# Kernel tuning notes

Hardware: AMD Instinct MI355X
Metric: run time of the kernel (lower is better)

Reference implementation:

```python
import jax, jax.numpy as jnp
import numpy as np

B, TXT_T, MEL_T, N_MEL = 8, 200, 800, 80
PAD_MAG = 1.0e12


def setup_inputs() -> dict:
    key = jax.random.key(0)
    k1, k2, k3, k4 = jax.random.split(key, 4)
    mu_logvar = jax.random.normal(k1, (B, TXT_T, 2 * N_MEL), dtype=jnp.float32)
    melspec = jax.random.normal(k2, (B, N_MEL, MEL_T), dtype=jnp.float32)
    # lengths are 1-based (indexed as length-1), keep them in [T//2, T]
    text_lengths = jax.random.randint(k3, (B,), TXT_T // 2, TXT_T + 1)
    mel_lengths = jax.random.randint(k4, (B,), MEL_T // 2, MEL_T + 1)
    return {
        "mu_logvar": mu_logvar,
        "melspec": melspec,
        "text_lengths": text_lengths,
        "mel_lengths": mel_lengths,
    }


def _log_prob_matrix(mu_logvar, melspec):
    # melspec: [B, n_mel, mel_T] -> x: [B, 1, mel_T, n_mel]
    x = jnp.transpose(melspec, (0, 2, 1))[:, None, :, :]
    mu = mu_logvar[:, :, :N_MEL][:, :, None, :]       # [B, txt_T, 1, n_mel]
    logvar = mu_logvar[:, :, N_MEL:][:, :, None, :]   # [B, txt_T, 1, n_mel]
    # -0.5 * mean_over_mel( (x-mu)^2 / exp(logvar) + logvar )
    sq = (x - mu) ** 2
    return (-0.5 * (sq * jnp.exp(-logvar) + logvar)).mean(axis=3)  # [B, txt_T, mel_T]


def reference(mu_logvar, melspec, text_lengths, mel_lengths):
    lp = _log_prob_matrix(mu_logvar, melspec)  # [B, txt_T, mel_T]

    # log_alpha column carry, with a leading pad row (index 0 stays -PAD_MAG)
    init = jnp.full((B, TXT_T + 1), -PAD_MAG, dtype=lp.dtype)
    init = init.at[:, 1].set(lp[:, 0, 0])

    def step(a, lp_t):  # a: [B, txt_T+1], lp_t: [B, txt_T]
        # logsumexp over {stay, advance}; original adds 1e-7 to prev values
        new_rows = jnp.logaddexp(a[:, 1:] + 1e-7, a[:, :-1] + 1e-7) + lp_t
        a = a.at[:, 1:].set(new_rows)
        return a, new_rows

    lp_rest = jnp.moveaxis(lp[:, :, 1:], 2, 0)  # [mel_T-1, B, txt_T]
    _, cols = jax.lax.scan(step, init, lp_rest)  # cols: [mel_T-1, B, txt_T]

    log_alpha = jnp.concatenate(
        [init[:, 1:, None], jnp.moveaxis(cols, 0, 2)], axis=2
    )  # [B, txt_T, mel_T]

    b = jnp.arange(B)
    alpha_last = log_alpha[b, text_lengths - 1, mel_lengths - 1]
    alpha_last = alpha_last / mel_lengths.astype(alpha_last.dtype)
    mdn_loss = -alpha_last.mean()
    return mdn_loss, lp
```

## Files before the change

kernel.cpp:

```cpp
#include <hip/hip_runtime.h>
#include <math.h>

#define BB 8
#define TXT_T 200
#define MEL_T 800
#define N_MEL 80
#define NTHR 192
#define LOG2E 1.44269504088896340736f
#define LN2   0.69314718055994530942f
#define EPS2  (1e-7f * LOG2E)
#define NPAD  -1.0e12f

__device__ __forceinline__ float exp2_hw(float x) {
#if __has_builtin(__builtin_amdgcn_exp2f)
    return __builtin_amdgcn_exp2f(x);
#else
    return __expf(LN2 * x);
#endif
}

__device__ __forceinline__ float lse2(float A, float B) {
    float m = fmaxf(A, B);
    float e = exp2_hw(-fabsf(A - B));
    return m + __log2f(1.0f + e);
}

template <int D>
__device__ __forceinline__ float dpp_shr(float v, float old) {
#if __has_builtin(__builtin_amdgcn_update_dpp)
    return __int_as_float(__builtin_amdgcn_update_dpp(
        __float_as_int(old), __float_as_int(v), 0x110 | D, 0xF, 0xF, false));
#else
    float t = __shfl_up(v, D);
    return ((threadIdx.x & 15) < D) ? old : t;
#endif
}

__global__ void __launch_bounds__(256) lp_kernel(
        const float* __restrict__ mu_logvar,
        const float* __restrict__ melspec,
        float* __restrict__ out_lp,
        float* __restrict__ lpT) {
    const int bt = blockIdx.x;
    const int b  = bt / TXT_T;
    const int tid = threadIdx.x;

    __shared__ float s_mu[N_MEL];
    __shared__ float s_ev[N_MEL];
    __shared__ float s_lv[N_MEL];
    __shared__ float s_sumlv;

    if (tid < N_MEL) {
        float mu = mu_logvar[(size_t)bt * (2 * N_MEL) + tid];
        float lv = mu_logvar[(size_t)bt * (2 * N_MEL) + N_MEL + tid];
        s_mu[tid] = mu;
        s_ev[tid] = __expf(-lv);
        s_lv[tid] = lv;
    }
    __syncthreads();
    if (tid == 0) {
        float s = 0.f;
        #pragma unroll
        for (int n = 0; n < N_MEL; ++n) s += s_lv[n];
        s_sumlv = s;
    }
    __syncthreads();

    if (tid < MEL_T / 4) {
        const float4* ms4 = (const float4*)(melspec + (size_t)b * N_MEL * MEL_T);
        float ax = 0.f, ay = 0.f, az = 0.f, aw = 0.f;
        #pragma unroll 8
        for (int n = 0; n < N_MEL; ++n) {
            float4 x = ms4[(size_t)n * (MEL_T / 4) + tid];
            float mu = s_mu[n];
            float ev = s_ev[n];
            float d0 = x.x - mu; ax += d0 * d0 * ev;
            float d1 = x.y - mu; ay += d1 * d1 * ev;
            float d2 = x.z - mu; az += d2 * d2 * ev;
            float d3 = x.w - mu; aw += d3 * d3 * ev;
        }
        const float c = -0.5f / (float)N_MEL;
        float slv = s_sumlv;
        float l0 = c * (ax + slv);
        float l1 = c * (ay + slv);
        float l2 = c * (az + slv);
        float l3 = c * (aw + slv);

        size_t ob = (size_t)bt * MEL_T + tid * 4;
        out_lp[ob + 0] = l0;
        out_lp[ob + 1] = l1;
        out_lp[ob + 2] = l2;
        out_lp[ob + 3] = l3;

        float4 v;
        v.x = l0 * LOG2E + EPS2;
        v.y = l1 * LOG2E + EPS2;
        v.z = l2 * LOG2E + EPS2;
        v.w = l3 * LOG2E + EPS2;
        *(float4*)(lpT + ob) = v;
    }
}

__global__ void __launch_bounds__(NTHR) scan_kernel(
        const float* __restrict__ lpT,
        const int* __restrict__ text_lengths,
        const int* __restrict__ mel_lengths,
        float* __restrict__ alpha_out) {
    __shared__ float tot[2][4][2];
    const int b = blockIdx.x;
    const int tid = threadIdx.x;
    const int w = tid >> 6;
    const int lane = tid & 63;

    const int melL1 = mel_lengths[b] - 1;
    const int txtL1 = text_lengths[b] - 1;
    const float scale = LN2 / (float)(melL1 + 1);
    const int estar = melL1 - txtL1;
    const int gtid = estar >> 2;
    const int gk = estar & 3;

    const float* cb = lpT + (size_t)b * TXT_T * MEL_T;

    float A0 = (tid == 0) ? -EPS2 : NPAD;
    float A1 = NPAD, A2 = NPAD, A3 = NPAD;

    #define LDCOL(JN, L0, L1, L2, L3) do {                                    \
        int jn_ = (JN);                                                       \
        const float* cp_ = cb + (size_t)jn_ * MEL_T;                          \
        int t0_ = jn_ + 4 * tid;                                              \
        int i0_ = t0_ + 0 > 799 ? 799 : t0_ + 0;                              \
        int i1_ = t0_ + 1 > 799 ? 799 : t0_ + 1;                              \
        int i2_ = t0_ + 2 > 799 ? 799 : t0_ + 2;                              \
        int i3_ = t0_ + 3 > 799 ? 799 : t0_ + 3;                              \
        L0 = cp_[i0_]; L1 = cp_[i1_]; L2 = cp_[i2_]; L3 = cp_[i3_];           \
    } while (0)

    float p0, p1, p2, p3, n0, n1, n2, n3;
    LDCOL(0, p0, p1, p2, p3);
    LDCOL(txtL1 >= 1 ? 1 : 0, n0, n1, n2, n3);

    int par = 0;
    for (int j = 0; j <= txtL1; ++j) {
        float al0 = p0, al1 = p1, al2 = p2, al3 = p3;
        p0 = n0; p1 = n1; p2 = n2; p3 = n3;
        {
            int jn = j + 2 > txtL1 ? txtL1 : j + 2;
            LDCOL(jn, n0, n1, n2, n3);
        }

        float be0 = al0 + A0;
        float be1 = al1 + A1;
        float be2 = al2 + A2;
        float be3 = al3 + A3;

        float I0a = al0,        I0b = be0;
        float I1a = al1 + I0a,  I1b = lse2(al1 + I0b, be1);
        float t23a = al3 + al2, t23b = lse2(al3 + be2, be3);
        float I2a = al2 + I1a,  I2b = lse2(al2 + I1b, be2);
        float I3a = t23a + I1a, I3b = lse2(t23a + I1b, t23b);

        float Ta = I3a, Tb = I3b;
        {
            float ia, ib;
            ia = dpp_shr<1>(Ta, 0.0f); ib = dpp_shr<1>(Tb, NPAD);
            Tb = lse2(Ta + ib, Tb); Ta = Ta + ia;
            ia = dpp_shr<2>(Ta, 0.0f); ib = dpp_shr<2>(Tb, NPAD);
            Tb = lse2(Ta + ib, Tb); Ta = Ta + ia;
            ia = dpp_shr<4>(Ta, 0.0f); ib = dpp_shr<4>(Tb, NPAD);
            Tb = lse2(Ta + ib, Tb); Ta = Ta + ia;
            ia = dpp_shr<8>(Ta, 0.0f); ib = dpp_shr<8>(Tb, NPAD);
            Tb = lse2(Ta + ib, Tb); Ta = Ta + ia;
        }

        float t0a = __shfl(Ta, 15), t0b = __shfl(Tb, 15);
        float t1a = __shfl(Ta, 31), t1b = __shfl(Tb, 31);
        float t2a = __shfl(Ta, 47), t2b = __shfl(Tb, 47);
        float c2a = t1a + t0a, c2b = lse2(t1a + t0b, t1b);
        float c3a = t2a + c2a, c3b = lse2(t2a + c2b, t2b);
        int row = lane >> 4;
        float Xa = 0.0f, Xb = NPAD;
        if (row == 1) { Xa = t0a; Xb = t0b; }
        if (row == 2) { Xa = c2a; Xb = c2b; }
        if (row == 3) { Xa = c3a; Xb = c3b; }
        float Fa = Ta + Xa;
        float Fb = lse2(Ta + Xb, Tb);

        float pfa = __shfl_up(Fa, 1);
        float pfb = __shfl_up(Fb, 1);
        if (lane == 63) { tot[par][w][0] = Fa; tot[par][w][1] = Fb; }
        asm volatile("s_waitcnt lgkmcnt(0)" ::: "memory");
        asm volatile("s_barrier" ::: "memory");

        float Wxa = 0.0f, Wxb = NPAD;
        if (w >= 1) { Wxa = tot[par][0][0]; Wxb = tot[par][0][1]; }
        if (w >= 2) {
            float ga = tot[par][1][0], gb = tot[par][1][1];
            Wxb = lse2(ga + Wxb, gb);
            Wxa = ga + Wxa;
        }

        float Exb;
        if (lane == 0) Exb = Wxb;
        else           Exb = lse2(pfa + Wxb, pfb);

        float B0 = lse2(I0a + Exb, I0b);
        float B1 = lse2(I1a + Exb, I1b);
        float B2 = lse2(I2a + Exb, I2b);
        float B3 = lse2(I3a + Exb, I3b);

        if (j == txtL1 && tid == gtid) {
            float g = B0;
            if (gk == 1) g = B1;
            if (gk == 2) g = B2;
            if (gk == 3) g = B3;
            alpha_out[b] = g * scale;
        }

        A0 = B0; A1 = B1; A2 = B2; A3 = B3;
        par ^= 1;
    }
}

__global__ void finish_kernel(const float* __restrict__ alpha,
                              float* __restrict__ out) {
    float s = 0.f;
    #pragma unroll
    for (int b = 0; b < BB; ++b) s += alpha[b];
    out[0] = -(s / (float)BB);
}

extern "C" void kernel_launch(void* const* d_in, const int* in_sizes, int n_in,
                              void* d_out, int out_size, void* d_ws, size_t ws_size,
                              hipStream_t stream) {
    const float* mu_logvar    = (const float*)d_in[0];
    const float* melspec      = (const float*)d_in[1];
    const int*   text_lengths = (const int*)d_in[2];
    const int*   mel_lengths  = (const int*)d_in[3];
    float* out = (float*)d_out;

    float* alpha = (float*)d_ws;
    float* lpT   = (float*)d_ws + 64;

    lp_kernel<<<BB * TXT_T, 256, 0, stream>>>(mu_logvar, melspec, out + 1, lpT);
    scan_kernel<<<BB, NTHR, 0, stream>>>(lpT, text_lengths, mel_lengths, alpha);
    finish_kernel<<<1, 1, 0, stream>>>(alpha, out);
}
```

Baseline: 127.5 us.

## Stage scan columns into LDS via async global_load_lds double buffering

```diff
diff --git a/kernel.cpp b/kernel.cpp
--- a/kernel.cpp
+++ b/kernel.cpp
@@ -6,6 +6,7 @@
 #define MEL_T 800
 #define N_MEL 80
 #define NTHR 192
+#define CSTR 1024
 #define LOG2E 1.44269504088896340736f
 #define LN2   0.69314718055994530942f
 #define EPS2  (1e-7f * LOG2E)
@@ -97,8 +98,19 @@
         v.y = l1 * LOG2E + EPS2;
         v.z = l2 * LOG2E + EPS2;
         v.w = l3 * LOG2E + EPS2;
-        *(float4*)(lpT + ob) = v;
-    }
+        *(float4*)(lpT + (size_t)bt * CSTR + tid * 4) = v;
+    } else {
+        float4 zz; zz.x = 0.f; zz.y = 0.f; zz.z = 0.f; zz.w = 0.f;
+        *(float4*)(lpT + (size_t)bt * CSTR + 800 + (tid - 200) * 4) = zz;
+    }
+}
+
+__device__ __forceinline__ void stage_col(const float* row, float* sb,
+                                          int w, int lane) {
+    __builtin_amdgcn_global_load_lds(
+        (const __attribute__((address_space(1))) void*)(row + w * 256 + lane * 4),
+        (__attribute__((address_space(3))) void*)(sb + w * 256),
+        16, 0, 0);
 }
 
 __global__ void __launch_bounds__(NTHR) scan_kernel(
@@ -106,6 +118,7 @@
         const int* __restrict__ text_lengths,
         const int* __restrict__ mel_lengths,
         float* __restrict__ alpha_out) {
+    __shared__ float sbuf[2][784];
     __shared__ float tot[2][4][2];
     const int b = blockIdx.x;
     const int tid = threadIdx.x;
@@ -119,34 +132,29 @@
     const int gtid = estar >> 2;
     const int gk = estar & 3;
 
-    const float* cb = lpT + (size_t)b * TXT_T * MEL_T;
+    const float* cb = lpT + (size_t)b * TXT_T * CSTR;
+
+    if (tid < 16) { sbuf[0][768 + tid] = 0.0f; sbuf[1][768 + tid] = 0.0f; }
+    asm volatile("s_waitcnt lgkmcnt(0)" ::: "memory");
 
     float A0 = (tid == 0) ? -EPS2 : NPAD;
     float A1 = NPAD, A2 = NPAD, A3 = NPAD;
 
-    #define LDCOL(JN, L0, L1, L2, L3) do {                                    \
-        int jn_ = (JN);                                                       \
-        const float* cp_ = cb + (size_t)jn_ * MEL_T;                          \
-        int t0_ = jn_ + 4 * tid;                                              \
-        int i0_ = t0_ + 0 > 799 ? 799 : t0_ + 0;                              \
-        int i1_ = t0_ + 1 > 799 ? 799 : t0_ + 1;                              \
-        int i2_ = t0_ + 2 > 799 ? 799 : t0_ + 2;                              \
-        int i3_ = t0_ + 3 > 799 ? 799 : t0_ + 3;                              \
-        L0 = cp_[i0_]; L1 = cp_[i1_]; L2 = cp_[i2_]; L3 = cp_[i3_];           \
-    } while (0)
-
-    float p0, p1, p2, p3, n0, n1, n2, n3;
-    LDCOL(0, p0, p1, p2, p3);
-    LDCOL(txtL1 >= 1 ? 1 : 0, n0, n1, n2, n3);
+    stage_col(cb, &sbuf[0][0], w, lane);
+    stage_col(cb + (size_t)1 * CSTR + 0, &sbuf[1][0], w, lane);
 
     int par = 0;
     for (int j = 0; j <= txtL1; ++j) {
-        float al0 = p0, al1 = p1, al2 = p2, al3 = p3;
-        p0 = n0; p1 = n1; p2 = n2; p3 = n3;
-        {
-            int jn = j + 2 > txtL1 ? txtL1 : j + 2;
-            LDCOL(jn, n0, n1, n2, n3);
-        }
+        asm volatile("s_waitcnt vmcnt(1)" ::: "memory");
+        __builtin_amdgcn_sched_barrier(0);
+        asm volatile("s_barrier" ::: "memory");
+
+        const float* sb = &sbuf[par][0];
+        const int off = (j & 3) + 4 * tid;
+        float al0 = sb[off + 0];
+        float al1 = sb[off + 1];
+        float al2 = sb[off + 2];
+        float al3 = sb[off + 3];
 
         float be0 = al0 + A0;
         float be1 = al1 + A1;
@@ -177,11 +185,11 @@
         float t2a = __shfl(Ta, 47), t2b = __shfl(Tb, 47);
         float c2a = t1a + t0a, c2b = lse2(t1a + t0b, t1b);
         float c3a = t2a + c2a, c3b = lse2(t2a + c2b, t2b);
-        int row = lane >> 4;
+        int row_ = lane >> 4;
         float Xa = 0.0f, Xb = NPAD;
-        if (row == 1) { Xa = t0a; Xb = t0b; }
-        if (row == 2) { Xa = c2a; Xb = c2b; }
-        if (row == 3) { Xa = c3a; Xb = c3b; }
+        if (row_ == 1) { Xa = t0a; Xb = t0b; }
+        if (row_ == 2) { Xa = c2a; Xb = c2b; }
+        if (row_ == 3) { Xa = c3a; Xb = c3b; }
         float Fa = Ta + Xa;
         float Fb = lse2(Ta + Xb, Tb);
 
@@ -190,6 +198,12 @@
         if (lane == 63) { tot[par][w][0] = Fa; tot[par][w][1] = Fb; }
         asm volatile("s_waitcnt lgkmcnt(0)" ::: "memory");
         asm volatile("s_barrier" ::: "memory");
+
+        {
+            int jn = j + 2; if (jn > txtL1) jn = txtL1;
+            stage_col(cb + (size_t)jn * CSTR + (jn & ~3), &sbuf[par][0],
+                      w, lane);
+        }
 
         float Wxa = 0.0f, Wxb = NPAD;
         if (w >= 1) { Wxa = tot[par][0][0]; Wxb = tot[par][0][1]; }
@@ -219,6 +233,7 @@
         A0 = B0; A1 = B1; A2 = B2; A3 = B3;
         par ^= 1;
     }
+    asm volatile("s_waitcnt vmcnt(0)" ::: "memory");
 }
 
 __global__ void finish_kernel(const float* __restrict__ alpha,
```

Result: slower. 142.8 us (+12.0%).
